# Optimization experiments

Measured on AMD Instinct MI355X. Metric: run time of the kernel, lower is better.

Reference implementation:

```python
import jax, jax.numpy as jnp
import numpy as np

RATIO = 0.5  # SAGPooling ratio


def setup_inputs() -> dict:
    key = jax.random.key(0)
    ks = jax.random.split(key, 6)
    B, n, d, out_dim, Eg = 128, 512, 256, 256, 4096  # graphs, nodes/graph, feat, proj out, edges/graph
    N = B * n
    x = jax.random.normal(ks[0], (N, d), dtype=jnp.float32)
    # edges connect nodes within the same graph (contiguous node blocks)
    src = jax.random.randint(ks[1], (B, Eg), 0, n)
    dst = jax.random.randint(ks[2], (B, Eg), 0, n)
    off = (jnp.arange(B) * n)[:, None]
    edge_index = jnp.stack([(src + off).reshape(-1), (dst + off).reshape(-1)]).astype(jnp.int32)
    batch = jnp.repeat(jnp.arange(B), n).astype(jnp.int32)
    s = 1.0 / np.sqrt(d).astype(np.float32)
    w_rel = jax.random.normal(ks[3], (d, 1), dtype=jnp.float32) * s   # GraphConv lin_rel (has bias)
    b_rel = jnp.zeros((1,), dtype=jnp.float32)
    w_root = jax.random.normal(ks[4], (d, 1), dtype=jnp.float32) * s  # GraphConv lin_root (no bias)
    w_proj = jax.random.normal(ks[5], (d, out_dim), dtype=jnp.float32) * s  # projection Linear
    b_proj = jnp.zeros((out_dim,), dtype=jnp.float32)
    return {"x": x, "edge_index": edge_index, "batch": batch, "num_graphs": B,
            "w_rel": w_rel, "b_rel": b_rel, "w_root": w_root,
            "w_proj": w_proj, "b_proj": b_proj}


def reference(x, edge_index, batch, num_graphs, w_rel, b_rel, w_root, w_proj, b_proj):
    N, d = x.shape
    n = N // num_graphs                    # equal-size graphs
    k = int(np.ceil(RATIO * n))            # PyG topk: ceil(ratio * num_nodes)
    src, dst = edge_index[0], edge_index[1]
    # GraphConv(node_dim, 1): score_i = lin_rel(sum_{j->i} x_j) + lin_root(x_i)
    agg = jax.ops.segment_sum(x[src], dst, num_segments=N)          # [N, d]
    score = jnp.tanh((agg @ w_rel + b_rel + x @ w_root)[:, 0])       # [N], tanh nonlinearity
    sb = score.reshape(num_graphs, n)                                # [B, n]
    top_vals, top_idx = jax.lax.top_k(sb, k)                         # per-graph topk
    xb = x.reshape(num_graphs, n, d)
    x_sel = jnp.take_along_axis(xb, top_idx[:, :, None], axis=1)     # [B, k, d]
    x_sel = x_sel * top_vals[:, :, None]                             # x[perm] * score[perm] (multiplier=1)
    pooled = x_sel.mean(axis=1)                                      # global_mean_pool over k kept nodes
    return pooled @ w_proj + b_proj                                  # [B, out_dim]
```

## Files before the change

kernel.cpp:

```cpp
#include <hip/hip_runtime.h>

#define D        256
#define NPG      512
#define BG       128
#define KSEL     256
#define EPG      4096
#define NN       (BG * NPG)
#define ET       (BG * EPG)

__global__ __launch_bounds__(256) void k_proj_scores(
        const float* __restrict__ x,
        const float* __restrict__ w_rel, const float* __restrict__ w_root,
        float* __restrict__ p, float* __restrict__ r) {
    int tid  = threadIdx.x;
    int wave = tid >> 6, lane = tid & 63;
    int node = blockIdx.x * 4 + wave;

    const float4* x4  = (const float4*)(x + (size_t)node * D);
    float4 xv = x4[lane];
    float4 wr = ((const float4*)w_rel)[lane];
    float4 wo = ((const float4*)w_root)[lane];
    float pv = xv.x * wr.x + xv.y * wr.y + xv.z * wr.z + xv.w * wr.w;
    float rv = xv.x * wo.x + xv.y * wo.y + xv.z * wo.z + xv.w * wo.w;
    #pragma unroll
    for (int off = 32; off; off >>= 1) {
        pv += __shfl_xor(pv, off, 64);
        rv += __shfl_xor(rv, off, 64);
    }
    if (lane == 0) { p[node] = pv; r[node] = rv; }
}

__global__ __launch_bounds__(1024) void k_select_pool(
        const float* __restrict__ x, const int* __restrict__ ei,
        const float* __restrict__ p, const float* __restrict__ r,
        const float* __restrict__ b_rel,
        const float* __restrict__ w_proj, const float* __restrict__ b_proj,
        float* __restrict__ out) {
    __shared__ __align__(16) float s_p[NPG];
    __shared__ __align__(16) float s_agg[NPG];
    __shared__ __align__(16) float s_val[NPG];
    __shared__ int   s_cnt2[1024];
    __shared__ int   s_selid[KSEL];
    __shared__ __align__(16) float s_selv[KSEL];
    __shared__ __align__(16) float s_pool[D];
    __shared__ __align__(16) float s_red[16][D];
    __shared__ int   s_nsel;

    int b = blockIdx.x, tid = threadIdx.x;
    int wave = tid >> 6, lane = tid & 63;
    int base = b * NPG;

    if (tid < NPG) { s_p[tid] = p[base + tid]; s_agg[tid] = 0.f; }
    if (tid == 0)  s_nsel = 0;
    __syncthreads();

    {
        const int* src = ei + (size_t)b * EPG;
        const int* dst = ei + ET + (size_t)b * EPG;
        #pragma unroll
        for (int e = tid; e < EPG; e += 1024)
            atomicAdd(&s_agg[dst[e] - base], s_p[src[e] - base]);
    }
    __syncthreads();

    if (tid < NPG)
        s_val[tid] = tanhf(s_agg[tid] + b_rel[0] + r[base + tid]);
    __syncthreads();

    {
        int j = tid & (NPG - 1);
        int half = tid >> 9;
        float sv = s_val[j];
        int lo = half * (NPG / 2);
        const float4* v4 = (const float4*)(s_val + lo);
        int c = 0;
        #pragma unroll 8
        for (int q = 0; q < NPG / 8; ++q) {
            float4 o = v4[q];
            int i0 = lo + q * 4;
            c += (o.x > sv) || (o.x == sv && (i0 + 0) < j);
            c += (o.y > sv) || (o.y == sv && (i0 + 1) < j);
            c += (o.z > sv) || (o.z == sv && (i0 + 2) < j);
            c += (o.w > sv) || (o.w == sv && (i0 + 3) < j);
        }
        s_cnt2[tid] = c;
    }
    __syncthreads();
    if (tid < NPG) {
        int rank = s_cnt2[tid] + s_cnt2[tid + NPG];
        if (rank < KSEL) {
            int pos = atomicAdd(&s_nsel, 1);
            s_selid[pos] = tid;
            s_selv[pos]  = s_val[tid];
        }
    }
    __syncthreads();

    {
        float4 acc = {0.f, 0.f, 0.f, 0.f};
        #pragma unroll
        for (int m = 0; m < 16; ++m) {
            int s   = wave * 16 + m;
            int row = s_selid[s];
            float v = s_selv[s];
            float4 xv = ((const float4*)(x + (size_t)(base + row) * D))[lane];
            acc.x += v * xv.x; acc.y += v * xv.y;
            acc.z += v * xv.z; acc.w += v * xv.w;
        }
        ((float4*)s_red[wave])[lane] = acc;
    }
    __syncthreads();
    if (tid < D) {
        float s = 0.f;
        #pragma unroll
        for (int w = 0; w < 16; ++w) s += s_red[w][tid];
        s_pool[tid] = s;
    }
    __syncthreads();

    {
        int f = tid & (D - 1);
        int q = tid >> 8;
        const float4* pool4 = (const float4*)s_pool + q * 16;
        const float* wp = w_proj + (size_t)(q * 64) * D + f;
        float acc = 0.f;
        #pragma unroll
        for (int t = 0; t < 16; ++t) {
            float4 pv = pool4[t];
            acc += pv.x * wp[(t * 4 + 0) * D];
            acc += pv.y * wp[(t * 4 + 1) * D];
            acc += pv.z * wp[(t * 4 + 2) * D];
            acc += pv.w * wp[(t * 4 + 3) * D];
        }
        s_red[q][f] = acc;
    }
    __syncthreads();
    if (tid < D)
        out[(size_t)b * D + tid] = b_proj[tid] +
            (s_red[0][tid] + s_red[1][tid] + s_red[2][tid] + s_red[3][tid]) * (1.0f / KSEL);
}

extern "C" void kernel_launch(void* const* d_in, const int* in_sizes, int n_in,
                              void* d_out, int out_size, void* d_ws, size_t ws_size,
                              hipStream_t stream) {
    const float* x      = (const float*)d_in[0];
    const int*   ei     = (const int*)d_in[1];
    const float* w_rel  = (const float*)d_in[4];
    const float* b_rel  = (const float*)d_in[5];
    const float* w_root = (const float*)d_in[6];
    const float* w_proj = (const float*)d_in[7];
    const float* b_proj = (const float*)d_in[8];
    float* out = (float*)d_out;

    float* p = (float*)d_ws;
    float* r = p + NN;

    k_proj_scores<<<NN / 4, 256, 0, stream>>>(x, w_rel, w_root, p, r);
    k_select_pool<<<BG, 1024, 0, stream>>>(x, ei, p, r, b_rel, w_proj, b_proj, out);
}
```

Measured before the change: 135.6 us.

## Split per-graph select-pool across two blocks with last-block combine

Launches two blocks per graph. Each block still recomputes the edge aggregation and scores for the whole graph, then ranks only half of the nodes and pools and projects the selected rows from that half. A partial projection goes to workspace, and the last-arriving block (tracked by an atomic counter reset in the first kernel) sums the two halves and writes the output. The goal is better use of the GPU's CUs, since 128 blocks underfill the device. The cost is duplicated aggregation work, extra workspace traffic, and threadfence synchronisation.

```diff
diff --git a/kernel.cpp b/kernel.cpp
--- a/kernel.cpp
+++ b/kernel.cpp
@@ -11,8 +11,9 @@
 __global__ __launch_bounds__(256) void k_proj_scores(
         const float* __restrict__ x,
         const float* __restrict__ w_rel, const float* __restrict__ w_root,
-        float* __restrict__ p, float* __restrict__ r) {
+        float* __restrict__ p, float* __restrict__ r, int* __restrict__ cnt) {
     int tid  = threadIdx.x;
+    if (blockIdx.x == 0 && tid < BG) cnt[tid] = 0;
     int wave = tid >> 6, lane = tid & 63;
     int node = blockIdx.x * 4 + wave;
 
@@ -35,19 +36,22 @@
         const float* __restrict__ p, const float* __restrict__ r,
         const float* __restrict__ b_rel,
         const float* __restrict__ w_proj, const float* __restrict__ b_proj,
+        float* __restrict__ ppart, int* __restrict__ cnt,
         float* __restrict__ out) {
     __shared__ __align__(16) float s_p[NPG];
     __shared__ __align__(16) float s_agg[NPG];
     __shared__ __align__(16) float s_val[NPG];
-    __shared__ int   s_cnt2[1024];
-    __shared__ int   s_selid[KSEL];
-    __shared__ __align__(16) float s_selv[KSEL];
+    __shared__ int   s_cnt4[1024];
+    __shared__ int   s_selid[256];
+    __shared__ __align__(16) float s_selv[256];
     __shared__ __align__(16) float s_pool[D];
     __shared__ __align__(16) float s_red[16][D];
     __shared__ int   s_nsel;
+    __shared__ int   s_last;
 
-    int b = blockIdx.x, tid = threadIdx.x;
-    int wave = tid >> 6, lane = tid & 63;
+    int blk = blockIdx.x;
+    int b = blk >> 1, half = blk & 1;
+    int tid = threadIdx.x, wave = tid >> 6, lane = tid & 63;
     int base = b * NPG;
 
     if (tid < NPG) { s_p[tid] = p[base + tid]; s_agg[tid] = 0.f; }
@@ -68,39 +72,38 @@
     __syncthreads();
 
     {
-        int j = tid & (NPG - 1);
-        int half = tid >> 9;
+        int j = half * 256 + (tid & 255);
+        int q = tid >> 8;
         float sv = s_val[j];
-        int lo = half * (NPG / 2);
-        const float4* v4 = (const float4*)(s_val + lo);
+        const float4* v4 = (const float4*)s_val + q * 32;
+        int i0b = q * 128;
         int c = 0;
         #pragma unroll 8
-        for (int q = 0; q < NPG / 8; ++q) {
-            float4 o = v4[q];
-            int i0 = lo + q * 4;
+        for (int t = 0; t < 32; ++t) {
+            float4 o = v4[t];
+            int i0 = i0b + t * 4;
             c += (o.x > sv) || (o.x == sv && (i0 + 0) < j);
             c += (o.y > sv) || (o.y == sv && (i0 + 1) < j);
             c += (o.z > sv) || (o.z == sv && (i0 + 2) < j);
             c += (o.w > sv) || (o.w == sv && (i0 + 3) < j);
         }
-        s_cnt2[tid] = c;
+        s_cnt4[tid] = c;
     }
     __syncthreads();
-    if (tid < NPG) {
-        int rank = s_cnt2[tid] + s_cnt2[tid + NPG];
+    if (tid < 256) {
+        int rank = s_cnt4[tid] + s_cnt4[tid + 256] + s_cnt4[tid + 512] + s_cnt4[tid + 768];
         if (rank < KSEL) {
             int pos = atomicAdd(&s_nsel, 1);
-            s_selid[pos] = tid;
-            s_selv[pos]  = s_val[tid];
+            s_selid[pos] = half * 256 + tid;
+            s_selv[pos]  = s_val[half * 256 + tid];
         }
     }
     __syncthreads();
+    int nsel = s_nsel;
 
     {
         float4 acc = {0.f, 0.f, 0.f, 0.f};
-        #pragma unroll
-        for (int m = 0; m < 16; ++m) {
-            int s   = wave * 16 + m;
+        for (int s = wave; s < nsel; s += 16) {
             int row = s_selid[s];
             float v = s_selv[s];
             float4 xv = ((const float4*)(x + (size_t)(base + row) * D))[lane];
@@ -136,8 +139,21 @@
     }
     __syncthreads();
     if (tid < D)
-        out[(size_t)b * D + tid] = b_proj[tid] +
-            (s_red[0][tid] + s_red[1][tid] + s_red[2][tid] + s_red[3][tid]) * (1.0f / KSEL);
+        ppart[(size_t)blk * D + tid] =
+            s_red[0][tid] + s_red[1][tid] + s_red[2][tid] + s_red[3][tid];
+
+    __threadfence();
+    __syncthreads();
+    if (tid == 0) s_last = (atomicAdd(&cnt[b], 1) == 1);
+    __syncthreads();
+    if (s_last) {
+        __threadfence();
+        if (tid < D) {
+            float a = ppart[(size_t)(2 * b) * D + tid]
+                    + ppart[(size_t)(2 * b + 1) * D + tid];
+            out[(size_t)b * D + tid] = b_proj[tid] + a * (1.0f / KSEL);
+        }
+    }
 }
 
 extern "C" void kernel_launch(void* const* d_in, const int* in_sizes, int n_in,
@@ -152,9 +168,12 @@
     const float* b_proj = (const float*)d_in[8];
     float* out = (float*)d_out;
 
-    float* p = (float*)d_ws;
-    float* r = p + NN;
+    float* p     = (float*)d_ws;
+    float* r     = p + NN;
+    int*   cnt   = (int*)(r + NN);
+    float* ppart = (float*)(cnt + BG);
 
-    k_proj_scores<<<NN / 4, 256, 0, stream>>>(x, w_rel, w_root, p, r);
-    k_select_pool<<<BG, 1024, 0, stream>>>(x, ei, p, r, b_rel, w_proj, b_proj, out);
+    k_proj_scores<<<NN / 4, 256, 0, stream>>>(x, w_rel, w_root, p, r, cnt);
+    k_select_pool<<<2 * BG, 1024, 0, stream>>>(x, ei, p, r, b_rel,
+                                               w_proj, b_proj, ppart, cnt, out);
 }
```

Result: slower. 246.2 us (+81.5%).

## Split per-graph select/pool across four blocks with atomic pooling and separate projection

Applied to the files above, without the earlier changes.

Each graph's selection and pooling is now spread over four blocks, each ranking and gathering a quarter of the nodes. Partial pooled sums are combined with global atomics into a workspace buffer, which the first kernel zeroes. A new third kernel then runs the projection. This raises parallelism from 128 blocks to 512 on a GPU with many CUs. The cost is that each block redoes the edge aggregation and tanh scoring, and there is an extra kernel launch plus float atomics, which can make the summation order nondeterministic.

```diff
diff --git a/kernel.cpp b/kernel.cpp
--- a/kernel.cpp
+++ b/kernel.cpp
@@ -11,8 +11,10 @@
 __global__ __launch_bounds__(256) void k_proj_scores(
         const float* __restrict__ x,
         const float* __restrict__ w_rel, const float* __restrict__ w_root,
-        float* __restrict__ p, float* __restrict__ r) {
+        float* __restrict__ p, float* __restrict__ r,
+        float* __restrict__ pool) {
     int tid  = threadIdx.x;
+    if (blockIdx.x < BG) pool[(size_t)blockIdx.x * D + tid] = 0.f;
     int wave = tid >> 6, lane = tid & 63;
     int node = blockIdx.x * 4 + wave;
 
@@ -34,20 +36,19 @@
         const float* __restrict__ x, const int* __restrict__ ei,
         const float* __restrict__ p, const float* __restrict__ r,
         const float* __restrict__ b_rel,
-        const float* __restrict__ w_proj, const float* __restrict__ b_proj,
-        float* __restrict__ out) {
+        float* __restrict__ pool) {
     __shared__ __align__(16) float s_p[NPG];
     __shared__ __align__(16) float s_agg[NPG];
     __shared__ __align__(16) float s_val[NPG];
-    __shared__ int   s_cnt2[1024];
-    __shared__ int   s_selid[KSEL];
-    __shared__ __align__(16) float s_selv[KSEL];
-    __shared__ __align__(16) float s_pool[D];
+    __shared__ int   s_cnt[1024];
+    __shared__ int   s_selid[128];
+    __shared__ __align__(16) float s_selv[128];
     __shared__ __align__(16) float s_red[16][D];
     __shared__ int   s_nsel;
 
-    int b = blockIdx.x, tid = threadIdx.x;
-    int wave = tid >> 6, lane = tid & 63;
+    int blk = blockIdx.x;
+    int b = blk >> 2, quarter = blk & 3;
+    int tid = threadIdx.x, wave = tid >> 6, lane = tid & 63;
     int base = b * NPG;
 
     if (tid < NPG) { s_p[tid] = p[base + tid]; s_agg[tid] = 0.f; }
@@ -68,39 +69,41 @@
     __syncthreads();
 
     {
-        int j = tid & (NPG - 1);
-        int half = tid >> 9;
+        int jj = tid & 127;
+        int j  = quarter * 128 + jj;
+        int q  = tid >> 7;
         float sv = s_val[j];
-        int lo = half * (NPG / 2);
-        const float4* v4 = (const float4*)(s_val + lo);
+        const float4* v4 = (const float4*)s_val + q * 16;
+        int i0b = q * 64;
         int c = 0;
-        #pragma unroll 8
-        for (int q = 0; q < NPG / 8; ++q) {
-            float4 o = v4[q];
-            int i0 = lo + q * 4;
+        #pragma unroll
+        for (int t = 0; t < 16; ++t) {
+            float4 o = v4[t];
+            int i0 = i0b + t * 4;
             c += (o.x > sv) || (o.x == sv && (i0 + 0) < j);
             c += (o.y > sv) || (o.y == sv && (i0 + 1) < j);
             c += (o.z > sv) || (o.z == sv && (i0 + 2) < j);
             c += (o.w > sv) || (o.w == sv && (i0 + 3) < j);
         }
-        s_cnt2[tid] = c;
+        s_cnt[tid] = c;
     }
     __syncthreads();
-    if (tid < NPG) {
-        int rank = s_cnt2[tid] + s_cnt2[tid + NPG];
+    if (tid < 128) {
+        int rank = 0;
+        #pragma unroll
+        for (int m = 0; m < 8; ++m) rank += s_cnt[tid + m * 128];
         if (rank < KSEL) {
             int pos = atomicAdd(&s_nsel, 1);
-            s_selid[pos] = tid;
-            s_selv[pos]  = s_val[tid];
+            s_selid[pos] = quarter * 128 + tid;
+            s_selv[pos]  = s_val[quarter * 128 + tid];
         }
     }
     __syncthreads();
+    int nsel = s_nsel;
 
     {
         float4 acc = {0.f, 0.f, 0.f, 0.f};
-        #pragma unroll
-        for (int m = 0; m < 16; ++m) {
-            int s   = wave * 16 + m;
+        for (int s = wave; s < nsel; s += 16) {
             int row = s_selid[s];
             float v = s_selv[s];
             float4 xv = ((const float4*)(x + (size_t)(base + row) * D))[lane];
@@ -114,10 +117,19 @@
         float s = 0.f;
         #pragma unroll
         for (int w = 0; w < 16; ++w) s += s_red[w][tid];
-        s_pool[tid] = s;
+        atomicAdd(&pool[(size_t)b * D + tid], s);
     }
+}
+
+__global__ __launch_bounds__(1024) void k_project(
+        const float* __restrict__ pool,
+        const float* __restrict__ w_proj, const float* __restrict__ b_proj,
+        float* __restrict__ out) {
+    __shared__ __align__(16) float s_pool[D];
+    __shared__ __align__(16) float s_red[4][D];
+    int b = blockIdx.x, tid = threadIdx.x;
+    if (tid < D) s_pool[tid] = pool[(size_t)b * D + tid];
     __syncthreads();
-
     {
         int f = tid & (D - 1);
         int q = tid >> 8;
@@ -152,9 +164,11 @@
     const float* b_proj = (const float*)d_in[8];
     float* out = (float*)d_out;
 
-    float* p = (float*)d_ws;
-    float* r = p + NN;
+    float* p    = (float*)d_ws;
+    float* r    = p + NN;
+    float* pool = r + NN;
 
-    k_proj_scores<<<NN / 4, 256, 0, stream>>>(x, w_rel, w_root, p, r);
-    k_select_pool<<<BG, 1024, 0, stream>>>(x, ei, p, r, b_rel, w_proj, b_proj, out);
+    k_proj_scores<<<NN / 4, 256, 0, stream>>>(x, w_rel, w_root, p, r, pool);
+    k_select_pool<<<4 * BG, 1024, 0, stream>>>(x, ei, p, r, b_rel, pool);
+    k_project<<<BG, 1024, 0, stream>>>(pool, w_proj, b_proj, out);
 }
```

New measurement: 131.4 us. 1.03x faster.
